# Kernel optimization log

Hardware: AMD Instinct MI355X
Metric: run time of the kernel (lower is better)

## Reference

```python
import jax, jax.numpy as jnp
import numpy as np
import math

EPS = 1e-5      # artanh boundary clamp (Poincare ball)
MIN_NORM = 1e-15

def _norm(x):
    return jnp.clip(jnp.linalg.norm(x, axis=-1, keepdims=True), MIN_NORM, None)

def artanh(x):
    x = jnp.clip(x, -1.0 + EPS, 1.0 - EPS)
    return 0.5 * (jnp.log1p(x) - jnp.log1p(-x))

def expmap0(u):
    # c = 1 Poincare ball: tanh(||u||) * u / ||u||
    n = _norm(u)
    return jnp.tanh(n) * u / n

def mobius_matvec(M, x):
    # geoopt: mx = x @ M^T; res = tanh(||mx||/||x|| * artanh(||x||)) * mx/||mx||
    xn = _norm(x)
    mx = x @ M.T
    mxn = _norm(mx)
    res = jnp.tanh(mxn / xn * artanh(xn)) * mx / mxn
    zero_row = jnp.all(mx == 0, axis=-1, keepdims=True)
    return jnp.where(zero_row, jnp.zeros_like(res), res)

def mobius_add(x, y):
    x2 = jnp.sum(x * x, axis=-1, keepdims=True)
    y2 = jnp.sum(y * y, axis=-1, keepdims=True)
    xy = jnp.sum(x * y, axis=-1, keepdims=True)
    num = (1.0 + 2.0 * xy + y2) * x + (1.0 - x2) * y
    den = 1.0 + 2.0 * xy + x2 * y2
    return num / jnp.clip(den, MIN_NORM, None)

def dist(x, y):
    # d(x,y) = 2 * artanh(|| (-x) mobius+ y ||); reduces the last dim
    return 2.0 * artanh(_norm(mobius_add(-x, y)))[..., 0]

def setup_inputs() -> dict:
    key = jax.random.key(0)
    k1, k2, k3, k4, k5 = jax.random.split(key, 5)
    B, S, H, D = 64, 1024, 768, 64
    bound = 1.0 / math.sqrt(D)
    sequence_output = jax.random.normal(k1, (B, S, H), dtype=jnp.float32) * 0.1
    proj = jax.random.uniform(k2, (H, D), dtype=jnp.float32, minval=-0.05, maxval=0.05)
    trans = jax.random.uniform(k3, (D, D), dtype=jnp.float32, minval=-0.05, maxval=0.05)
    pos = expmap0(jax.random.uniform(k4, (D,), dtype=jnp.float32, minval=-bound, maxval=bound))
    neg = expmap0(jax.random.uniform(k5, (D,), dtype=jnp.float32, minval=-bound, maxval=bound))
    return {"sequence_output": sequence_output, "proj": proj, "trans": trans,
            "pos": pos, "neg": neg}

def reference(sequence_output, proj, trans, pos, neg):
    t = sequence_output @ proj          # [B, S, 64]
    t = expmap0(t)
    t = mobius_matvec(trans, t)
    pos_logits = dist(neg, t).sum(-1)   # [B]
    neg_logits = dist(pos, t).sum(-1)   # [B]
    return jnp.stack((neg_logits, pos_logits), axis=-1)  # [B, 2]
```

## Files before the change

### kernel.cpp

```cpp
#include <hip/hip_runtime.h>
#include <math.h>

#define MIN_NORM 1e-15f
#define BOUND_EPS 1e-5f

typedef __attribute__((ext_vector_type(8))) short short8v;
typedef __attribute__((ext_vector_type(4))) float f32x4;

__device__ __forceinline__ unsigned short f2bf(float f) {
  unsigned int u = __float_as_uint(f);
  unsigned int r = (u + 0x7FFFu + ((u >> 16) & 1u)) >> 16;
  return (unsigned short)r;
}

__device__ __forceinline__ float gred16(float v) {
  v += __shfl_xor(v, 1, 64);
  v += __shfl_xor(v, 2, 64);
  v += __shfl_xor(v, 4, 64);
  v += __shfl_xor(v, 8, 64);
  return v;
}
__device__ __forceinline__ float wred64(float v) {
#pragma unroll
  for (int off = 32; off; off >>= 1) v += __shfl_xor(v, off, 64);
  return v;
}
__device__ __forceinline__ float artanh_c(float x) {
  x = fminf(fmaxf(x, -1.f + BOUND_EPS), 1.f - BOUND_EPS);
  return 0.5f * logf((1.f + x) / (1.f - x));
}

__global__ __launch_bounds__(256) void poincare_prep(
    const float* __restrict__ proj, const float* __restrict__ trans,
    unsigned short* __restrict__ projB, unsigned short* __restrict__ transB) {
  int idx = blockIdx.x * 256 + threadIdx.x;
  if (idx < 49152) {
    int j = idx & 7, l = (idx >> 3) & 63, nt = (idx >> 9) & 3, kt = idx >> 11;
    projB[idx] = f2bf(proj[(kt * 32 + (l >> 4) * 8 + j) * 64 + nt * 16 + (l & 15)]);
  } else if (idx < 49152 + 4096) {
    int i2 = idx - 49152;
    int j = i2 & 7, l = (i2 >> 3) & 63, nt = (i2 >> 9) & 3, kt = i2 >> 11;
    transB[i2] = f2bf(trans[(nt * 16 + (l & 15)) * 64 + kt * 32 + (l >> 4) * 8 + j]);
  }
}

__global__ __launch_bounds__(512, 8) void poincare_main(
    const float* __restrict__ seq,
    const unsigned short* __restrict__ projB,
    const unsigned short* __restrict__ transB,
    const float* __restrict__ pos, const float* __restrict__ neg,
    float* __restrict__ wsPart) {
  __shared__ unsigned short teL[4][16 * 64];
  __shared__ float xbuf[4][64][17];
  __shared__ float partial[4][2];

  const int tid = threadIdx.x;
  const int w = tid >> 6, l = tid & 63;
  const int p = w & 3, h = w >> 2;
  const int lr = l & 15, lk = l >> 4;
  const long bIdx = blockIdx.x;

  const float* pA = seq + ((bIdx * 64 + p * 16 + lr) * 768 + h * 384 + lk * 8);
  const unsigned short* pB = projB + h * 12 * 2048 + l * 8;

  f32x4 acc[4];
#pragma unroll
  for (int nt = 0; nt < 4; ++nt) acc[nt] = (f32x4){0.f, 0.f, 0.f, 0.f};

  for (int kt = 0; kt < 12; ++kt) {
    float4 a0 = *(const float4*)(pA);
    float4 a1 = *(const float4*)(pA + 4);
    pA += 32;
    const unsigned short* pb = pB + kt * 2048;
    short8v b0 = *(const short8v*)(pb);
    short8v b1 = *(const short8v*)(pb + 512);
    short8v b2 = *(const short8v*)(pb + 1024);
    short8v b3 = *(const short8v*)(pb + 1536);
    short8v av;
    av[0] = (short)f2bf(a0.x); av[1] = (short)f2bf(a0.y);
    av[2] = (short)f2bf(a0.z); av[3] = (short)f2bf(a0.w);
    av[4] = (short)f2bf(a1.x); av[5] = (short)f2bf(a1.y);
    av[6] = (short)f2bf(a1.z); av[7] = (short)f2bf(a1.w);
    acc[0] = __builtin_amdgcn_mfma_f32_16x16x32_bf16(av, b0, acc[0], 0, 0, 0);
    acc[1] = __builtin_amdgcn_mfma_f32_16x16x32_bf16(av, b1, acc[1], 0, 0, 0);
    acc[2] = __builtin_amdgcn_mfma_f32_16x16x32_bf16(av, b2, acc[2], 0, 0, 0);
    acc[3] = __builtin_amdgcn_mfma_f32_16x16x32_bf16(av, b3, acc[3], 0, 0, 0);
  }

  if (h) {
#pragma unroll
    for (int nt = 0; nt < 4; ++nt)
#pragma unroll
      for (int i = 0; i < 4; ++i) xbuf[p][l][nt * 4 + i] = acc[nt][i];
  }
  __syncthreads();

  float th[4];
  if (!h) {
#pragma unroll
    for (int nt = 0; nt < 4; ++nt)
#pragma unroll
      for (int i = 0; i < 4; ++i) acc[nt][i] += xbuf[p][l][nt * 4 + i];

#pragma unroll
    for (int i = 0; i < 4; ++i) {
      float s = acc[0][i] * acc[0][i] + acc[1][i] * acc[1][i] +
                acc[2][i] * acc[2][i] + acc[3][i] * acc[3][i];
      s = gred16(s);
      float n = fmaxf(sqrtf(s), MIN_NORM);
      float t = tanhf(n);
      th[i] = fmaxf(t, MIN_NORM);
      float sc = t / n;
#pragma unroll
      for (int nt = 0; nt < 4; ++nt) acc[nt][i] *= sc;
    }

    unsigned short* buf = teL[p];
#pragma unroll
    for (int i = 0; i < 4; ++i) {
      int row = lk * 4 + i;
      int sw = (row & 7) << 3;
#pragma unroll
      for (int nt = 0; nt < 4; ++nt) {
        int col = nt * 16 + lr;
        buf[row * 64 + (col ^ sw)] = f2bf(acc[nt][i]);
      }
    }
  }
  __syncthreads();

  if (!h) {
    const unsigned short* buf = teL[p];
    f32x4 acc2[4];
#pragma unroll
    for (int nt = 0; nt < 4; ++nt) acc2[nt] = (f32x4){0.f, 0.f, 0.f, 0.f};
    const unsigned short* pT = transB + l * 8;
#pragma unroll
    for (int kt = 0; kt < 2; ++kt) {
      short8v a2 = *(const short8v*)&buf[lr * 64 + ((kt * 32 + lk * 8) ^ ((lr & 7) << 3))];
      const unsigned short* pt = pT + kt * 2048;
      short8v c0 = *(const short8v*)(pt);
      short8v c1 = *(const short8v*)(pt + 512);
      short8v c2 = *(const short8v*)(pt + 1024);
      short8v c3 = *(const short8v*)(pt + 1536);
      acc2[0] = __builtin_amdgcn_mfma_f32_16x16x32_bf16(a2, c0, acc2[0], 0, 0, 0);
      acc2[1] = __builtin_amdgcn_mfma_f32_16x16x32_bf16(a2, c1, acc2[1], 0, 0, 0);
      acc2[2] = __builtin_amdgcn_mfma_f32_16x16x32_bf16(a2, c2, acc2[2], 0, 0, 0);
      acc2[3] = __builtin_amdgcn_mfma_f32_16x16x32_bf16(a2, c3, acc2[3], 0, 0, 0);
    }

    float xp[4], xq[4];
#pragma unroll
    for (int nt = 0; nt < 4; ++nt) {
      xp[nt] = pos[nt * 16 + lr];
      xq[nt] = neg[nt * 16 + lr];
    }
    float x2p = wred64(xp[0] * xp[0] + xp[1] * xp[1] + xp[2] * xp[2] + xp[3] * xp[3]) * 0.25f;
    float x2n = wred64(xq[0] * xq[0] + xq[1] * xq[1] + xq[2] * xq[2] + xq[3] * xq[3]) * 0.25f;

    float distP = 0.f, distN = 0.f;
#pragma unroll
    for (int i = 0; i < 4; ++i) {
      float m0 = acc2[0][i], m1 = acc2[1][i], m2 = acc2[2][i], m3 = acc2[3][i];
      float s = gred16(m0 * m0 + m1 * m1 + m2 * m2 + m3 * m3);
      float mxn = fmaxf(sqrtf(s), MIN_NORM);
      float xn = th[i];
      float rs = tanhf(mxn / xn * artanh_c(xn)) / mxn;
      float r0 = rs * m0, r1 = rs * m1, r2 = rs * m2, r3 = rs * m3;
      float y2 = gred16(r0 * r0 + r1 * r1 + r2 * r2 + r3 * r3);
      float xyP = -gred16(xp[0] * r0 + xp[1] * r1 + xp[2] * r2 + xp[3] * r3);
      float xyN = -gred16(xq[0] * r0 + xq[1] * r1 + xq[2] * r2 + xq[3] * r3);
      {
        float A = 1.f + 2.f * xyP + y2, B = 1.f - x2p;
        float inv = 1.f / fmaxf(1.f + 2.f * xyP + x2p * y2, MIN_NORM);
        float v0 = (B * r0 - A * xp[0]) * inv, v1 = (B * r1 - A * xp[1]) * inv;
        float v2 = (B * r2 - A * xp[2]) * inv, v3 = (B * r3 - A * xp[3]) * inv;
        float nv = fmaxf(sqrtf(gred16(v0 * v0 + v1 * v1 + v2 * v2 + v3 * v3)), MIN_NORM);
        distP += 2.f * artanh_c(nv);
      }
      {
        float A = 1.f + 2.f * xyN + y2, B = 1.f - x2n;
        float inv = 1.f / fmaxf(1.f + 2.f * xyN + x2n * y2, MIN_NORM);
        float v0 = (B * r0 - A * xq[0]) * inv, v1 = (B * r1 - A * xq[1]) * inv;
        float v2 = (B * r2 - A * xq[2]) * inv, v3 = (B * r3 - A * xq[3]) * inv;
        float nv = fmaxf(sqrtf(gred16(v0 * v0 + v1 * v1 + v2 * v2 + v3 * v3)), MIN_NORM);
        distN += 2.f * artanh_c(nv);
      }
    }
    float tP = wred64(distP) * 0.0625f;
    float tN = wred64(distN) * 0.0625f;
    if (l == 0) { partial[p][0] = tP; partial[p][1] = tN; }
  }
  __syncthreads();
  if (tid == 0) {
    wsPart[bIdx * 2 + 0] = partial[0][0] + partial[1][0] + partial[2][0] + partial[3][0];
    wsPart[bIdx * 2 + 1] = partial[0][1] + partial[1][1] + partial[2][1] + partial[3][1];
  }
}

__global__ __launch_bounds__(128) void poincare_reduce(const float* __restrict__ wsPart,
                                                       float* __restrict__ out) {
  int t = threadIdx.x;
  int b = t >> 1, j = t & 1;
  float s = 0.f;
#pragma unroll
  for (int i = 0; i < 16; ++i) s += wsPart[(b * 16 + i) * 2 + j];
  out[b * 2 + j] = s;
}

extern "C" void kernel_launch(void* const* d_in, const int* in_sizes, int n_in,
                              void* d_out, int out_size, void* d_ws, size_t ws_size,
                              hipStream_t stream) {
  const float* seq = (const float*)d_in[0];
  const float* proj = (const float*)d_in[1];
  const float* trans = (const float*)d_in[2];
  const float* pos = (const float*)d_in[3];
  const float* neg = (const float*)d_in[4];

  unsigned short* projB = (unsigned short*)d_ws;
  unsigned short* transB = projB + 49152;
  float* wsPart = (float*)((char*)d_ws + 106496);
  float* out = (float*)d_out;

  poincare_prep<<<208, 256, 0, stream>>>(proj, trans, projB, transB);
  poincare_main<<<1024, 512, 0, stream>>>(seq, projB, transB, pos, neg, wsPart);
  poincare_reduce<<<1, 128, 0, stream>>>(wsPart, out);
}
```

Before: 53.59 us.

## Batch seq loads in main GEMM loop and coalesce prep and reduce accesses

The main GEMM loop now issues the seq float4 loads for four k-steps up front, raising memory-level parallelism on the dominant HBM stream, and the occupancy hint in launch bounds drops from 8 to 4 to leave room for the extra registers. The prep kernel now reads proj and trans linearly and scatters the bf16 writes, and the partial sums are stored per output column so the reduce kernel can use float4 loads. The main risk is lower occupancy hiding less latency, which could offset the gain from the batched loads.

```diff
diff --git a/kernel.cpp b/kernel.cpp
--- a/kernel.cpp
+++ b/kernel.cpp
@@ -35,16 +35,22 @@
     unsigned short* __restrict__ projB, unsigned short* __restrict__ transB) {
   int idx = blockIdx.x * 256 + threadIdx.x;
   if (idx < 49152) {
-    int j = idx & 7, l = (idx >> 3) & 63, nt = (idx >> 9) & 3, kt = idx >> 11;
-    projB[idx] = f2bf(proj[(kt * 32 + (l >> 4) * 8 + j) * 64 + nt * 16 + (l & 15)]);
+    int k = idx >> 6, d = idx & 63;
+    int kt = k >> 5, t5 = k & 31, lk = t5 >> 3, j = t5 & 7;
+    int nt = d >> 4, lr = d & 15;
+    int l = lk * 16 + lr;
+    projB[((kt * 4 + nt) * 64 + l) * 8 + j] = f2bf(proj[idx]);
   } else if (idx < 49152 + 4096) {
     int i2 = idx - 49152;
-    int j = i2 & 7, l = (i2 >> 3) & 63, nt = (i2 >> 9) & 3, kt = i2 >> 11;
-    transB[i2] = f2bf(trans[(nt * 16 + (l & 15)) * 64 + kt * 32 + (l >> 4) * 8 + j]);
-  }
-}
-
-__global__ __launch_bounds__(512, 8) void poincare_main(
+    int r = i2 >> 6, c = i2 & 63;
+    int nt = r >> 4, lr = r & 15;
+    int kt = c >> 5, lk = (c >> 3) & 3, j = c & 7;
+    int l = lk * 16 + lr;
+    transB[((kt * 4 + nt) * 64 + l) * 8 + j] = f2bf(trans[i2]);
+  }
+}
+
+__global__ __launch_bounds__(512, 4) void poincare_main(
     const float* __restrict__ seq,
     const unsigned short* __restrict__ projB,
     const unsigned short* __restrict__ transB,
@@ -67,24 +73,31 @@
 #pragma unroll
   for (int nt = 0; nt < 4; ++nt) acc[nt] = (f32x4){0.f, 0.f, 0.f, 0.f};
 
-  for (int kt = 0; kt < 12; ++kt) {
-    float4 a0 = *(const float4*)(pA);
-    float4 a1 = *(const float4*)(pA + 4);
-    pA += 32;
-    const unsigned short* pb = pB + kt * 2048;
-    short8v b0 = *(const short8v*)(pb);
-    short8v b1 = *(const short8v*)(pb + 512);
-    short8v b2 = *(const short8v*)(pb + 1024);
-    short8v b3 = *(const short8v*)(pb + 1536);
-    short8v av;
-    av[0] = (short)f2bf(a0.x); av[1] = (short)f2bf(a0.y);
-    av[2] = (short)f2bf(a0.z); av[3] = (short)f2bf(a0.w);
-    av[4] = (short)f2bf(a1.x); av[5] = (short)f2bf(a1.y);
-    av[6] = (short)f2bf(a1.z); av[7] = (short)f2bf(a1.w);
-    acc[0] = __builtin_amdgcn_mfma_f32_16x16x32_bf16(av, b0, acc[0], 0, 0, 0);
-    acc[1] = __builtin_amdgcn_mfma_f32_16x16x32_bf16(av, b1, acc[1], 0, 0, 0);
-    acc[2] = __builtin_amdgcn_mfma_f32_16x16x32_bf16(av, b2, acc[2], 0, 0, 0);
-    acc[3] = __builtin_amdgcn_mfma_f32_16x16x32_bf16(av, b3, acc[3], 0, 0, 0);
+  for (int kt = 0; kt < 12; kt += 4) {
+    float4 a[8];
+#pragma unroll
+    for (int u = 0; u < 4; ++u) {
+      a[2 * u]     = *(const float4*)(pA + 32 * u);
+      a[2 * u + 1] = *(const float4*)(pA + 32 * u + 4);
+    }
+    pA += 128;
+#pragma unroll
+    for (int u = 0; u < 4; ++u) {
+      const unsigned short* pb = pB + (kt + u) * 2048;
+      short8v b0 = *(const short8v*)(pb);
+      short8v b1 = *(const short8v*)(pb + 512);
+      short8v b2 = *(const short8v*)(pb + 1024);
+      short8v b3 = *(const short8v*)(pb + 1536);
+      short8v av;
+      av[0] = (short)f2bf(a[2 * u].x); av[1] = (short)f2bf(a[2 * u].y);
+      av[2] = (short)f2bf(a[2 * u].z); av[3] = (short)f2bf(a[2 * u].w);
+      av[4] = (short)f2bf(a[2 * u + 1].x); av[5] = (short)f2bf(a[2 * u + 1].y);
+      av[6] = (short)f2bf(a[2 * u + 1].z); av[7] = (short)f2bf(a[2 * u + 1].w);
+      acc[0] = __builtin_amdgcn_mfma_f32_16x16x32_bf16(av, b0, acc[0], 0, 0, 0);
+      acc[1] = __builtin_amdgcn_mfma_f32_16x16x32_bf16(av, b1, acc[1], 0, 0, 0);
+      acc[2] = __builtin_amdgcn_mfma_f32_16x16x32_bf16(av, b2, acc[2], 0, 0, 0);
+      acc[3] = __builtin_amdgcn_mfma_f32_16x16x32_bf16(av, b3, acc[3], 0, 0, 0);
+    }
   }
 
   if (h) {
@@ -193,8 +206,8 @@
   }
   __syncthreads();
   if (tid == 0) {
-    wsPart[bIdx * 2 + 0] = partial[0][0] + partial[1][0] + partial[2][0] + partial[3][0];
-    wsPart[bIdx * 2 + 1] = partial[0][1] + partial[1][1] + partial[2][1] + partial[3][1];
+    wsPart[0 * 1024 + bIdx] = partial[0][0] + partial[1][0] + partial[2][0] + partial[3][0];
+    wsPart[1 * 1024 + bIdx] = partial[0][1] + partial[1][1] + partial[2][1] + partial[3][1];
   }
 }
 
@@ -202,9 +215,10 @@
                                                        float* __restrict__ out) {
   int t = threadIdx.x;
   int b = t >> 1, j = t & 1;
+  const float4* v = (const float4*)(wsPart + j * 1024 + b * 16);
   float s = 0.f;
 #pragma unroll
-  for (int i = 0; i < 16; ++i) s += wsPart[(b * 16 + i) * 2 + j];
+  for (int i = 0; i < 4; ++i) s += v[i].x + v[i].y + v[i].z + v[i].w;
   out[b * 2 + j] = s;
 }
 
```

Result: slower. 55.09 us (+2.8%).
